# Performance work log

Measured on AMD Instinct MI355X. Metric: run time of the kernel, lower is better.

## Reference

```python
import jax, jax.numpy as jnp
import numpy as np

NDCG_CUTOFF = 10
N_ITEMS = 8192


def setup_inputs() -> dict:
    key = jax.random.key(0)
    k1, k2 = jax.random.split(key)
    outputs = jax.random.normal(k1, (N_ITEMS, 1), dtype=jnp.float32)
    scores = jax.random.uniform(k2, (N_ITEMS, 1), dtype=jnp.float32)
    return {"outputs": outputs, "scores": scores}


def reference(outputs, scores):
    cutoff = NDCG_CUTOFF
    o = outputs[:, 0]  # [n]
    s = scores[:, 0]   # [n]
    n = o.shape[0]

    # rank of each item under descending sort of outputs (0-indexed)
    order = jnp.argsort(-o)
    ranks = jnp.zeros(n, dtype=jnp.int32).at[order].set(jnp.arange(n, dtype=jnp.int32))
    # discount D(r) = 1/log2(r+2) inside the NDCG cutoff, 0 outside
    disc = jnp.where(ranks < cutoff, 1.0 / jnp.log2(ranks.astype(jnp.float32) + 2.0), 0.0)

    gains = jnp.exp2(s) - 1.0  # 2^score - 1
    top_gains, _ = jax.lax.top_k(gains, cutoff)
    idcg = jnp.sum(top_gains / jnp.log2(jnp.arange(2, cutoff + 2, dtype=jnp.float32)))

    # swap-based delta-NDCG: swapping outputs i<->j swaps their ranks only
    # |delta_ndcg_ij| = |(g_i - g_j) * (D_i - D_j)| / IDCG
    delta = jnp.abs((gains[:, None] - gains[None, :]) * (disc[:, None] - disc[None, :])) / idcg
    # original skips pairs with equal outputs (their delta is 0 anyway)
    delta = jnp.where(o[:, None] != o[None, :], delta, 0.0)

    diff = o[:, None] - o[None, :]                       # [n,n] logits pre-sigmoid
    labels = (s[:, None] > s[None, :]).astype(o.dtype)   # [n,n]
    # BCE(sigmoid(diff), labels), numerically stable:
    # -log sigmoid(d) = softplus(-d); -log(1-sigmoid(d)) = softplus(d)
    bce = labels * jax.nn.softplus(-diff) + (1.0 - labels) * jax.nn.softplus(diff)

    loss = jnp.sum(bce * delta) / n
    return loss
```

## Files before the change

### kernel.cpp

```cpp
#include <hip/hip_runtime.h>
#include <math.h>
#include <stdint.h>

#define CUT  10
#define N    8192

#define WS_PART(ws) ((double*)(ws))
#define WS_OV(ws)   ((float*)((char*)(ws) + 256))
#define WS_GV(ws)   ((float*)((char*)(ws) + 296))
#define WS_INV(ws)  ((float*)((char*)(ws) + 336))
#define WS_OI(ws)   ((int*)((char*)(ws) + 344))

__device__ __forceinline__ uint64_t pack_key(float v, int i) {
    uint32_t fb = __float_as_uint(v);
    uint32_t k  = (fb & 0x80000000u) ? ~fb : (fb | 0x80000000u);
    return ((uint64_t)k << 32) | (uint32_t)~(uint32_t)i;
}
__device__ __forceinline__ float key_val(uint64_t key) {
    uint32_t k  = (uint32_t)(key >> 32);
    uint32_t fb = (k & 0x80000000u) ? (k & 0x7FFFFFFFu) : ~k;
    return __uint_as_float(fb);
}
__device__ __forceinline__ int key_idx(uint64_t key) {
    return (int)~(uint32_t)key;
}

#define B1    1024
#define HALF  512
#define PERT  (N / HALF)
#define GW    8

__global__ __launch_bounds__(B1, 4)
void k_select(const float* __restrict__ og, const float* __restrict__ sg,
              void* __restrict__ ws)
{
    __shared__ uint64_t wmax[2][2][GW];
    __shared__ int      sh_oi[CUT];

    const int tid  = threadIdx.x;
    const int lane = tid & 63;
    const int grp  = tid >> 9;
    const int gtid = tid & (HALF - 1);
    const int gwid = gtid >> 6;

    const float* __restrict__ src = grp ? sg : og;
    float vals[PERT];
    #pragma unroll
    for (int k = 0; k < PERT; ++k) vals[k] = src[gtid + k * HALF];

    float idcg = 0.f;
    int   w_idx_prev = -1;
    for (int t = 0; t < CUT; ++t) {
        #pragma unroll
        for (int k = 0; k < PERT; ++k)
            if (gtid + k * HALF == w_idx_prev) vals[k] = -INFINITY;
        float bv = vals[0]; int bk = 0;
        #pragma unroll
        for (int k = 1; k < PERT; ++k)
            if (vals[k] > bv) { bv = vals[k]; bk = k; }
        uint64_t m = pack_key(bv, gtid + bk * HALF);
        #pragma unroll
        for (int off = 32; off; off >>= 1) {
            uint64_t o = __shfl_xor((unsigned long long)m, off);
            m = (o > m) ? o : m;
        }
        const int par = t & 1;
        if (lane == 0) wmax[grp][par][gwid] = m;
        __syncthreads();
        uint64_t w = wmax[grp][par][0];
        #pragma unroll
        for (int q = 1; q < GW; ++q) { uint64_t v = wmax[grp][par][q]; if (v > w) w = v; }
        const float wv = key_val(w);
        const int   wi = key_idx(w);
        if (grp == 0) {
            if (tid == 0) { WS_OV(ws)[t] = wv; WS_OI(ws)[t] = wi; sh_oi[t] = wi; }
        } else {
            idcg += (exp2f(wv) - 1.f) / log2f((float)(t + 2));
        }
        w_idx_prev = wi;
    }
    if (tid == HALF) WS_INV(ws)[0] = 1.f / idcg;
    __syncthreads();
    if (tid < CUT) WS_GV(ws)[tid] = exp2f(sg[sh_oi[tid]]) - 1.f;
}

#define B2 256
#define G2 (N / B2)

__global__ __launch_bounds__(B2)
void k_sweep(const float* __restrict__ og, const float* __restrict__ sg,
             void* __restrict__ ws)
{
    __shared__ double wpart[B2 / 64];
    const int tid = threadIdx.x;
    const int j   = blockIdx.x * B2 + tid;

    float t_ov[CUT], t_gv[CUT], t_disc[CUT]; int t_oi[CUT];
    #pragma unroll
    for (int t = 0; t < CUT; ++t) {
        t_ov[t]   = WS_OV(ws)[t];
        t_gv[t]   = WS_GV(ws)[t];
        t_oi[t]   = WS_OI(ws)[t];
        t_disc[t] = 1.f / log2f((float)(t + 2));
    }
    const float inv_idcg = WS_INV(ws)[0];

    const float oj = og[j];
    const float gj = exp2f(sg[j]) - 1.f;
    int pos = CUT; float discj = 0.f;
    #pragma unroll
    for (int t = 0; t < CUT; ++t)
        if (t_oi[t] == j) { pos = t; discj = t_disc[t]; }

    double acc = 0.0;
    #pragma unroll
    for (int t = 0; t < CUT; ++t) {
        const float oi = t_ov[t];
        const float dg = t_gv[t] - gj;
        const float dd = t_disc[t] - discj;
        const float delta = fabsf(dg * dd) * inv_idcg;
        const float darg  = copysignf(1.f, dg) * (oj - oi);
        const float e  = exp2f(-fabsf(darg) * 1.4426950408889634f);
        const float l  = log2f(1.f + e);
        const float sp = fmaxf(darg, 0.f) + l * 0.6931471805599453f;
        if (t < pos && oi != oj)
            acc += (double)(delta * (2.f * sp));
    }
    #pragma unroll
    for (int off = 32; off; off >>= 1) acc += __shfl_down(acc, off);
    const int lane = tid & 63, wid = tid >> 6;
    if (lane == 0) wpart[wid] = acc;
    __syncthreads();
    if (tid == 0) {
        double tot = 0.0;
        #pragma unroll
        for (int w = 0; w < B2 / 64; ++w) tot += wpart[w];
        WS_PART(ws)[blockIdx.x] = tot;
    }
}

__global__ __launch_bounds__(64)
void k_final(void* __restrict__ ws, float* __restrict__ out)
{
    const int lane = threadIdx.x;
    double v = (lane < G2) ? WS_PART(ws)[lane] : 0.0;
    #pragma unroll
    for (int off = 32; off; off >>= 1) v += __shfl_down(v, off);
    if (lane == 0) out[0] = (float)(v / (double)N);
}

extern "C" void kernel_launch(void* const* d_in, const int* in_sizes, int n_in,
                              void* d_out, int out_size, void* d_ws, size_t ws_size,
                              hipStream_t stream) {
    const float* o = (const float*)d_in[0];
    const float* s = (const float*)d_in[1];
    float* out = (float*)d_out;
    k_select<<<dim3(1),  dim3(B1), 0, stream>>>(o, s, d_ws);
    k_sweep <<<dim3(G2), dim3(B2), 0, stream>>>(o, s, d_ws);
    k_final <<<dim3(1),  dim3(64), 0, stream>>>(d_ws, out);
}
```

Before: 74.88 us.

## Fuse select, sweep and final reduction into one single-block kernel

Merges the top-k selection, the pairwise sweep and the final reduction into one 1024-thread single-block kernel. The top-10 values, gains and inverse IDCG now pass through shared memory instead of a global workspace. Each thread then loops over 8 items. This removes two kernel launches and the global round-trips between them, at the cost of running the sweep on one CU instead of 32 blocks.

```diff
diff --git a/kernel.cpp b/kernel.cpp
--- a/kernel.cpp
+++ b/kernel.cpp
@@ -2,14 +2,14 @@
 #include <math.h>
 #include <stdint.h>
 
-#define CUT  10
-#define N    8192
-
-#define WS_PART(ws) ((double*)(ws))
-#define WS_OV(ws)   ((float*)((char*)(ws) + 256))
-#define WS_GV(ws)   ((float*)((char*)(ws) + 296))
-#define WS_INV(ws)  ((float*)((char*)(ws) + 336))
-#define WS_OI(ws)   ((int*)((char*)(ws) + 344))
+#define CUT   10
+#define N     8192
+#define B1    1024
+#define HALF  512
+#define PERT  (N / HALF)
+#define GW    8
+#define JPT   (N / B1)
+#define NWAVE (B1 / 64)
 
 __device__ __forceinline__ uint64_t pack_key(float v, int i) {
     uint32_t fb = __float_as_uint(v);
@@ -25,20 +25,21 @@
     return (int)~(uint32_t)key;
 }
 
-#define B1    1024
-#define HALF  512
-#define PERT  (N / HALF)
-#define GW    8
-
 __global__ __launch_bounds__(B1, 4)
-void k_select(const float* __restrict__ og, const float* __restrict__ sg,
-              void* __restrict__ ws)
+void lambdarank_fused(const float* __restrict__ og,
+                      const float* __restrict__ sg,
+                      float* __restrict__ out)
 {
     __shared__ uint64_t wmax[2][2][GW];
-    __shared__ int      sh_oi[CUT];
+    __shared__ float  sh_ov[CUT];
+    __shared__ int    sh_oi[CUT];
+    __shared__ float  sh_gv[CUT];
+    __shared__ float  sh_inv;
+    __shared__ double wpart[NWAVE];
 
     const int tid  = threadIdx.x;
     const int lane = tid & 63;
+    const int wid  = tid >> 6;
     const int grp  = tid >> 9;
     const int gtid = tid & (HALF - 1);
     const int gwid = gtid >> 6;
@@ -49,11 +50,11 @@
     for (int k = 0; k < PERT; ++k) vals[k] = src[gtid + k * HALF];
 
     float idcg = 0.f;
-    int   w_idx_prev = -1;
+    int   w_prev = -1;
     for (int t = 0; t < CUT; ++t) {
         #pragma unroll
         for (int k = 0; k < PERT; ++k)
-            if (gtid + k * HALF == w_idx_prev) vals[k] = -INFINITY;
+            if (gtid + k * HALF == w_prev) vals[k] = -INFINITY;
         float bv = vals[0]; int bk = 0;
         #pragma unroll
         for (int k = 1; k < PERT; ++k)
@@ -62,7 +63,7 @@
         #pragma unroll
         for (int off = 32; off; off >>= 1) {
             uint64_t o = __shfl_xor((unsigned long long)m, off);
-            m = (o > m) ? o : m;
+            if (o > m) m = o;
         }
         const int par = t & 1;
         if (lane == 0) wmax[grp][par][gwid] = m;
@@ -73,80 +74,62 @@
         const float wv = key_val(w);
         const int   wi = key_idx(w);
         if (grp == 0) {
-            if (tid == 0) { WS_OV(ws)[t] = wv; WS_OI(ws)[t] = wi; sh_oi[t] = wi; }
+            if (tid == 0) { sh_ov[t] = wv; sh_oi[t] = wi; }
         } else {
             idcg += (exp2f(wv) - 1.f) / log2f((float)(t + 2));
         }
-        w_idx_prev = wi;
+        w_prev = wi;
     }
-    if (tid == HALF) WS_INV(ws)[0] = 1.f / idcg;
+    if (tid == HALF) sh_inv = 1.f / idcg;
     __syncthreads();
-    if (tid < CUT) WS_GV(ws)[tid] = exp2f(sg[sh_oi[tid]]) - 1.f;
-}
-
-#define B2 256
-#define G2 (N / B2)
-
-__global__ __launch_bounds__(B2)
-void k_sweep(const float* __restrict__ og, const float* __restrict__ sg,
-             void* __restrict__ ws)
-{
-    __shared__ double wpart[B2 / 64];
-    const int tid = threadIdx.x;
-    const int j   = blockIdx.x * B2 + tid;
+    if (tid < CUT) sh_gv[tid] = exp2f(sg[sh_oi[tid]]) - 1.f;
+    __syncthreads();
 
     float t_ov[CUT], t_gv[CUT], t_disc[CUT]; int t_oi[CUT];
     #pragma unroll
     for (int t = 0; t < CUT; ++t) {
-        t_ov[t]   = WS_OV(ws)[t];
-        t_gv[t]   = WS_GV(ws)[t];
-        t_oi[t]   = WS_OI(ws)[t];
+        t_ov[t]   = sh_ov[t];
+        t_gv[t]   = sh_gv[t];
+        t_oi[t]   = sh_oi[t];
         t_disc[t] = 1.f / log2f((float)(t + 2));
     }
-    const float inv_idcg = WS_INV(ws)[0];
-
-    const float oj = og[j];
-    const float gj = exp2f(sg[j]) - 1.f;
-    int pos = CUT; float discj = 0.f;
-    #pragma unroll
-    for (int t = 0; t < CUT; ++t)
-        if (t_oi[t] == j) { pos = t; discj = t_disc[t]; }
+    const float inv_idcg = sh_inv;
 
     double acc = 0.0;
-    #pragma unroll
-    for (int t = 0; t < CUT; ++t) {
-        const float oi = t_ov[t];
-        const float dg = t_gv[t] - gj;
-        const float dd = t_disc[t] - discj;
-        const float delta = fabsf(dg * dd) * inv_idcg;
-        const float darg  = copysignf(1.f, dg) * (oj - oi);
-        const float e  = exp2f(-fabsf(darg) * 1.4426950408889634f);
-        const float l  = log2f(1.f + e);
-        const float sp = fmaxf(darg, 0.f) + l * 0.6931471805599453f;
-        if (t < pos && oi != oj)
-            acc += (double)(delta * (2.f * sp));
+    #pragma unroll 1
+    for (int k = 0; k < JPT; ++k) {
+        const int j  = tid + k * B1;
+        const float oj = og[j];
+        const float gj = exp2f(sg[j]) - 1.f;
+        int pos = CUT; float discj = 0.f;
+        #pragma unroll
+        for (int t = 0; t < CUT; ++t)
+            if (t_oi[t] == j) { pos = t; discj = t_disc[t]; }
+        #pragma unroll
+        for (int t = 0; t < CUT; ++t) {
+            const float oi = t_ov[t];
+            const float dg = t_gv[t] - gj;
+            const float dd = t_disc[t] - discj;
+            const float delta = fabsf(dg * dd) * inv_idcg;
+            const float darg  = copysignf(1.f, dg) * (oj - oi);
+            const float e  = exp2f(-fabsf(darg) * 1.4426950408889634f);
+            const float l  = log2f(1.f + e);
+            const float sp = fmaxf(darg, 0.f) + l * 0.6931471805599453f;
+            if (t < pos && oi != oj)
+                acc += (double)(delta * (2.f * sp));
+        }
     }
+
     #pragma unroll
     for (int off = 32; off; off >>= 1) acc += __shfl_down(acc, off);
-    const int lane = tid & 63, wid = tid >> 6;
     if (lane == 0) wpart[wid] = acc;
     __syncthreads();
     if (tid == 0) {
         double tot = 0.0;
         #pragma unroll
-        for (int w = 0; w < B2 / 64; ++w) tot += wpart[w];
-        WS_PART(ws)[blockIdx.x] = tot;
+        for (int w = 0; w < NWAVE; ++w) tot += wpart[w];
+        out[0] = (float)(tot / (double)N);
     }
-}
-
-__global__ __launch_bounds__(64)
-void k_final(void* __restrict__ ws, float* __restrict__ out)
-{
-    const int lane = threadIdx.x;
-    double v = (lane < G2) ? WS_PART(ws)[lane] : 0.0;
-    #pragma unroll
-    for (int off = 32; off; off >>= 1) v += __shfl_down(v, off);
-    if (lane == 0) out[0] = (float)(v / (double)N);
 }
 
 extern "C" void kernel_launch(void* const* d_in, const int* in_sizes, int n_in,
@@ -155,7 +138,5 @@
     const float* o = (const float*)d_in[0];
     const float* s = (const float*)d_in[1];
     float* out = (float*)d_out;
-    k_select<<<dim3(1),  dim3(B1), 0, stream>>>(o, s, d_ws);
-    k_sweep <<<dim3(G2), dim3(B2), 0, stream>>>(o, s, d_ws);
-    k_final <<<dim3(1),  dim3(64), 0, stream>>>(d_ws, out);
+    lambdarank_fused<<<dim3(1), dim3(B1), 0, stream>>>(o, s, out);
 }
```

After: 89.08 us. 1.19x slower.

## Split top-k selection into parallel per-chunk candidates plus single-block merge

Applied to the files above, without the earlier changes.

Replaces the single 1024-thread block that ran ten serial block-wide argmax rounds with two kernels. The first uses 32 one-wave blocks, each pulling the top-10 packed keys from a 512-element chunk using only wave shuffles. The second merges the 160 candidates per array in one 128-thread block. This removes the __syncthreads-heavy serial selection but adds a fourth kernel launch and a global round trip for the candidates.

```diff
diff --git a/kernel.cpp b/kernel.cpp
--- a/kernel.cpp
+++ b/kernel.cpp
@@ -10,6 +10,7 @@
 #define WS_GV(ws)   ((float*)((char*)(ws) + 296))
 #define WS_INV(ws)  ((float*)((char*)(ws) + 336))
 #define WS_OI(ws)   ((int*)((char*)(ws) + 344))
+#define WS_CAND(ws) ((uint64_t*)((char*)(ws) + 512))
 
 __device__ __forceinline__ uint64_t pack_key(float v, int i) {
     uint32_t fb = __float_as_uint(v);
@@ -25,63 +26,76 @@
     return (int)~(uint32_t)key;
 }
 
-#define B1    1024
-#define HALF  512
-#define PERT  (N / HALF)
-#define GW    8
+__global__ __launch_bounds__(64)
+void k_cand(const float* __restrict__ og, const float* __restrict__ sg,
+            void* __restrict__ ws)
+{
+    const int lane = threadIdx.x;
+    const int b    = blockIdx.x;
+    const int grp  = b >> 4;
+    const int cb   = b & 15;
+    const float* __restrict__ src = grp ? sg : og;
+    const int base = cb * 512;
 
-__global__ __launch_bounds__(B1, 4)
-void k_select(const float* __restrict__ og, const float* __restrict__ sg,
-              void* __restrict__ ws)
-{
-    __shared__ uint64_t wmax[2][2][GW];
-    __shared__ int      sh_oi[CUT];
+    uint64_t reg[8];
+    #pragma unroll
+    for (int k = 0; k < 8; ++k) {
+        const int i = base + lane + 64 * k;
+        reg[k] = pack_key(src[i], i);
+    }
+    uint64_t* __restrict__ outc = WS_CAND(ws) + grp * 160 + cb * CUT;
 
-    const int tid  = threadIdx.x;
-    const int lane = tid & 63;
-    const int grp  = tid >> 9;
-    const int gtid = tid & (HALF - 1);
-    const int gwid = gtid >> 6;
-
-    const float* __restrict__ src = grp ? sg : og;
-    float vals[PERT];
-    #pragma unroll
-    for (int k = 0; k < PERT; ++k) vals[k] = src[gtid + k * HALF];
-
-    float idcg = 0.f;
-    int   w_idx_prev = -1;
     for (int t = 0; t < CUT; ++t) {
+        uint64_t m = reg[0];
         #pragma unroll
-        for (int k = 0; k < PERT; ++k)
-            if (gtid + k * HALF == w_idx_prev) vals[k] = -INFINITY;
-        float bv = vals[0]; int bk = 0;
-        #pragma unroll
-        for (int k = 1; k < PERT; ++k)
-            if (vals[k] > bv) { bv = vals[k]; bk = k; }
-        uint64_t m = pack_key(bv, gtid + bk * HALF);
+        for (int k = 1; k < 8; ++k) if (reg[k] > m) m = reg[k];
         #pragma unroll
         for (int off = 32; off; off >>= 1) {
             uint64_t o = __shfl_xor((unsigned long long)m, off);
-            m = (o > m) ? o : m;
+            if (o > m) m = o;
         }
-        const int par = t & 1;
-        if (lane == 0) wmax[grp][par][gwid] = m;
-        __syncthreads();
-        uint64_t w = wmax[grp][par][0];
+        if (lane == 0) outc[t] = m;
         #pragma unroll
-        for (int q = 1; q < GW; ++q) { uint64_t v = wmax[grp][par][q]; if (v > w) w = v; }
-        const float wv = key_val(w);
-        const int   wi = key_idx(w);
-        if (grp == 0) {
-            if (tid == 0) { WS_OV(ws)[t] = wv; WS_OI(ws)[t] = wi; sh_oi[t] = wi; }
+        for (int k = 0; k < 8; ++k) if (reg[k] == m) reg[k] = 0;
+    }
+}
+
+__global__ __launch_bounds__(128)
+void k_merge(const float* __restrict__ sg, void* __restrict__ ws)
+{
+    const int tid  = threadIdx.x;
+    const int lane = tid & 63;
+    const int wv   = tid >> 6;
+    const uint64_t* __restrict__ cand = WS_CAND(ws) + wv * 160;
+
+    uint64_t c0 = cand[lane];
+    uint64_t c1 = cand[64 + lane];
+    uint64_t c2 = (lane < 32) ? cand[128 + lane] : 0;
+
+    float idcg = 0.f;
+    for (int t = 0; t < CUT; ++t) {
+        uint64_t m = c0;
+        if (c1 > m) m = c1;
+        if (c2 > m) m = c2;
+        #pragma unroll
+        for (int off = 32; off; off >>= 1) {
+            uint64_t o = __shfl_xor((unsigned long long)m, off);
+            if (o > m) m = o;
+        }
+        if (wv == 0) {
+            if (lane == 0) { WS_OV(ws)[t] = key_val(m); WS_OI(ws)[t] = key_idx(m); }
         } else {
-            idcg += (exp2f(wv) - 1.f) / log2f((float)(t + 2));
+            idcg += (exp2f(key_val(m)) - 1.f) / log2f((float)(t + 2));
         }
-        w_idx_prev = wi;
+        if (c0 == m) c0 = 0;
+        if (c1 == m) c1 = 0;
+        if (c2 == m) c2 = 0;
     }
-    if (tid == HALF) WS_INV(ws)[0] = 1.f / idcg;
-    __syncthreads();
-    if (tid < CUT) WS_GV(ws)[tid] = exp2f(sg[sh_oi[tid]]) - 1.f;
+    if (wv == 0 && lane == 0) {
+        for (int t = 0; t < CUT; ++t)
+            WS_GV(ws)[t] = exp2f(sg[WS_OI(ws)[t]]) - 1.f;
+    }
+    if (wv == 1 && lane == 0) WS_INV(ws)[0] = 1.f / idcg;
 }
 
 #define B2 256
@@ -155,7 +169,8 @@
     const float* o = (const float*)d_in[0];
     const float* s = (const float*)d_in[1];
     float* out = (float*)d_out;
-    k_select<<<dim3(1),  dim3(B1), 0, stream>>>(o, s, d_ws);
-    k_sweep <<<dim3(G2), dim3(B2), 0, stream>>>(o, s, d_ws);
-    k_final <<<dim3(1),  dim3(64), 0, stream>>>(d_ws, out);
+    k_cand <<<dim3(32), dim3(64),  0, stream>>>(o, s, d_ws);
+    k_merge<<<dim3(1),  dim3(128), 0, stream>>>(s, d_ws);
+    k_sweep<<<dim3(G2), dim3(B2),  0, stream>>>(o, s, d_ws);
+    k_final<<<dim3(1),  dim3(64),  0, stream>>>(d_ws, out);
 }
```

Measured after the change: 70.69 us. 1.06x faster.
